# Performance work log

Hardware: AMD Instinct MI355X
Metric: run time of the kernel (lower is better)

## Reference

```python
import jax, jax.numpy as jnp
import numpy as np

N = 50000      # nodes
E = 800000     # edges
IN = 30        # atom features
H = 8          # attention heads
D = 32         # per-head out feats
G = 512        # graphs in batch
HID = 128      # predictor hidden
TASKS = 1
ALPHA = 0.2    # LeakyReLU slope
BN_EPS = 1e-5


def setup_inputs() -> dict:
    key = jax.random.key(0)
    ks = jax.random.split(key, 20)
    f = lambda k, shp: (jax.random.normal(k, shp, dtype=jnp.float32) * 0.1)
    return {
        'x': jax.random.normal(ks[0], (N, IN), dtype=jnp.float32),
        'src': jax.random.randint(ks[1], (E,), 0, N, dtype=jnp.int32),
        'dst': jax.random.randint(ks[2], (E,), 0, N, dtype=jnp.int32),
        'graph_ids': jnp.sort(jax.random.randint(ks[3], (N,), 0, G, dtype=jnp.int32)),
        # GAT layer 1 (in=30 -> 8 heads x 32, flatten + ELU, residual projection)
        'W1': f(ks[4], (IN, H * D)),
        'al1': f(ks[5], (H, D)),
        'ar1': f(ks[6], (H, D)),
        'b1': jnp.zeros((H * D,), jnp.float32),
        'resW1': f(ks[7], (IN, H * D)),
        # GAT layer 2 (in=256 -> 8 heads x 32, mean over heads, identity residual)
        'W2': f(ks[8], (H * D, H * D)),
        'al2': f(ks[9], (H, D)),
        'ar2': f(ks[10], (H, D)),
        'b2': jnp.zeros((H * D,), jnp.float32),
        # WeightedSumAndMax readout gate
        'Ww': f(ks[11], (D, 1)),
        'bw': jnp.zeros((1,), jnp.float32),
        # MLP predictor: Linear -> ReLU -> BatchNorm(eval) -> Linear
        'Wp1': f(ks[12], (2 * D, HID)),
        'bp1': jnp.zeros((HID,), jnp.float32),
        'gamma': jnp.ones((HID,), jnp.float32),
        'beta': jnp.zeros((HID,), jnp.float32),
        'rm': jnp.zeros((HID,), jnp.float32),
        'rv': jnp.ones((HID,), jnp.float32),
        'Wp2': f(ks[13], (HID, TASKS)),
        'bp2': jnp.zeros((TASKS,), jnp.float32),
    }


def _gat_layer(h, src, dst, W, al, ar, b):
    # h: [N, F_in] -> out: [N, H, D]
    n = h.shape[0]
    feat = (h @ W).reshape(n, H, D)                    # projected features
    el = jnp.sum(feat * al, axis=-1)                   # [N, H]
    er = jnp.sum(feat * ar, axis=-1)                   # [N, H]
    e = el[src] + er[dst]                              # [E, H]
    e = jnp.where(e > 0, e, ALPHA * e)                 # LeakyReLU
    m = jax.ops.segment_max(e, dst, num_segments=n)    # segment-softmax max
    m = jnp.where(jnp.isfinite(m), m, 0.0)             # guard empty segments
    ex = jnp.exp(e - m[dst])                           # [E, H]
    s = jax.ops.segment_sum(ex, dst, num_segments=n)   # [N, H]
    a = ex / jnp.maximum(s[dst], 1e-9)                 # normalized attention
    msg = a[:, :, None] * feat[src]                    # [E, H, D]
    out = jax.ops.segment_sum(msg, dst, num_segments=n)
    return out + b.reshape(1, H, D)


def reference(x, src, dst, graph_ids, W1, al1, ar1, b1, resW1,
              W2, al2, ar2, b2, Ww, bw, Wp1, bp1, gamma, beta, rm, rv, Wp2, bp2):
    # Layer 1: residual projection (in_feats != H*D), flatten heads, ELU
    h1 = _gat_layer(x, src, dst, W1, al1, ar1, b1)
    h1 = h1 + (x @ resW1).reshape(N, H, D)
    h1 = jax.nn.elu(h1.reshape(N, H * D))
    # Layer 2: identity residual (in_feats == H*D), mean over heads, no activation
    h2 = _gat_layer(h1, src, dst, W2, al2, ar2, b2)
    h2 = h2 + h1.reshape(N, H, D)
    h2 = jnp.mean(h2, axis=1)                          # [N, D]
    # WeightedSumAndMax readout
    w = jax.nn.sigmoid(h2 @ Ww + bw)                   # [N, 1]
    gsum = jax.ops.segment_sum(w * h2, graph_ids, num_segments=G)
    gmax = jax.ops.segment_max(h2, graph_ids, num_segments=G)
    gmax = jnp.where(jnp.isfinite(gmax), gmax, 0.0)
    g = jnp.concatenate([gsum, gmax], axis=-1)         # [G, 2D]
    # MLP predictor (eval-mode BatchNorm)
    p = jax.nn.relu(g @ Wp1 + bp1)
    p = (p - rm) / jnp.sqrt(rv + BN_EPS) * gamma + beta
    return p @ Wp2 + bp2                               # [G, TASKS]
```

## Files before the change

kernel.cpp:

```cpp
#include <hip/hip_runtime.h>
#include <math.h>

#define NN 50000
#define EE 800000
#define IN_F 30
#define NH 8
#define DH 32
#define HD 256
#define NG 512
#define NHID 128
#define ALPHA 0.2f
#define ENC_NEG_INF 0x007fffffu

#define SCAN_B 256
#define SCAN_NB ((NN + SCAN_B - 1)/SCAN_B)

typedef unsigned short u16;

__device__ __forceinline__ u16 f2bf(float f){
  unsigned u = __float_as_uint(f);
  u = u + 0x7FFFu + ((u >> 16) & 1u);
  return (u16)(u >> 16);
}
__device__ __forceinline__ float bf2f(u16 b){
  return __uint_as_float(((unsigned)b) << 16);
}
__device__ __forceinline__ float4 bf4_to_f4(ushort4 v){
  float4 r; r.x=bf2f(v.x); r.y=bf2f(v.y); r.z=bf2f(v.z); r.w=bf2f(v.w); return r;
}

__device__ __forceinline__ unsigned encf(float x){
  unsigned u = __float_as_uint(x);
  return (u & 0x80000000u) ? ~u : (u | 0x80000000u);
}
__device__ __forceinline__ float decf(unsigned u){
  return (u & 0x80000000u) ? __uint_as_float(u & 0x7fffffffu) : __uint_as_float(~u);
}

__global__ void k_init(int* counts, float* gsum, unsigned* gmax){
  int i = blockIdx.x*blockDim.x + threadIdx.x;
  if(i < NN) counts[i] = 0;
  if(i < NG*DH){ gsum[i] = 0.f; gmax[i] = ENC_NEG_INF; }
}

__global__ void k_hist(const int* __restrict__ dst, int* counts){
  int i = blockIdx.x*blockDim.x + threadIdx.x;
  if(i < EE) atomicAdd(&counts[dst[i]], 1);
}

__global__ void k_scan_partial(const int* __restrict__ counts, int* __restrict__ bsums){
  __shared__ int sd[SCAN_B];
  int b = blockIdx.x, t = threadIdx.x;
  int idx = b*SCAN_B + t;
  sd[t] = (idx<NN)? counts[idx] : 0;
  __syncthreads();
  for(int off=SCAN_B/2; off>0; off>>=1){
    if(t<off) sd[t] += sd[t+off];
    __syncthreads();
  }
  if(t==0) bsums[b] = sd[0];
}

__global__ void k_scan_bsums(int* bsums){
  __shared__ int sd[SCAN_B];
  int t = threadIdx.x;
  int v = (t<SCAN_NB)? bsums[t] : 0;
  sd[t]=v; __syncthreads();
  for(int off=1; off<SCAN_B; off<<=1){
    int u = (t>=off)? sd[t-off] : 0;
    __syncthreads();
    sd[t] += u;
    __syncthreads();
  }
  if(t<SCAN_NB) bsums[t] = sd[t]-v;
}

__global__ void k_scan_final(const int* __restrict__ counts, const int* __restrict__ bsums,
                             int* __restrict__ start, int* __restrict__ cursor){
  __shared__ int sd[SCAN_B];
  int b = blockIdx.x, t = threadIdx.x;
  int idx = b*SCAN_B + t;
  int v = (idx<NN)? counts[idx] : 0;
  sd[t]=v; __syncthreads();
  for(int off=1; off<SCAN_B; off<<=1){
    int u = (t>=off)? sd[t-off] : 0;
    __syncthreads();
    sd[t] += u;
    __syncthreads();
  }
  int ex = sd[t]-v + bsums[b];
  if(idx<NN){ start[idx]=ex; cursor[idx]=ex; }
}

__global__ void k_scatter(const int* __restrict__ dst, const int* __restrict__ src,
                          int* cursor, int* __restrict__ csr_src){
  int i = blockIdx.x*blockDim.x + threadIdx.x;
  if(i<EE){ int p = atomicAdd(&cursor[dst[i]],1); csr_src[p]=src[i]; }
}

#define TM1 16
__global__ void k_proj1(const float* __restrict__ x, const float* __restrict__ W1,
                        u16* __restrict__ feat16){
  __shared__ float xs[TM1][IN_F];
  int n0 = blockIdx.x*TM1;
  int t = threadIdx.x;
  for(int i=t;i<TM1*IN_F;i+=256){
    int m=i/IN_F, k=i-m*IN_F;
    xs[m][k] = x[(size_t)(n0+m)*IN_F+k];
  }
  __syncthreads();
  int jq = (t & 63) << 2;
  int m0 = t >> 6;
  float4 acc[4];
  #pragma unroll
  for(int r=0;r<4;r++){ acc[r].x=0.f; acc[r].y=0.f; acc[r].z=0.f; acc[r].w=0.f; }
  for(int k=0;k<IN_F;k++){
    float4 w = *(const float4*)&W1[k*HD + jq];
    #pragma unroll
    for(int r=0;r<4;r++){
      float xv = xs[m0 + (r<<2)][k];
      acc[r].x += xv*w.x; acc[r].y += xv*w.y; acc[r].z += xv*w.z; acc[r].w += xv*w.w;
    }
  }
  #pragma unroll
  for(int r=0;r<4;r++){
    int n = n0 + m0 + (r<<2);
    ushort4 o; o.x=f2bf(acc[r].x); o.y=f2bf(acc[r].y); o.z=f2bf(acc[r].z); o.w=f2bf(acc[r].w);
    *(ushort4*)&feat16[(size_t)n*HD + jq] = o;
  }
}

#define BM 64
#define BN 64
#define BK 16
#define LDP (BM+4)
__global__ void k_proj2(const float* __restrict__ X, const float* __restrict__ W,
                        u16* __restrict__ Y16){
  __shared__ float As[BK][LDP];
  __shared__ float Bs[BK][LDP];
  int t  = threadIdx.x;
  int tx = t & 15, ty = t >> 4;
  int n0 = blockIdx.x*BM;
  int c0 = blockIdx.y*BN;
  float acc[4][4];
  #pragma unroll
  for(int i=0;i<4;i++)
    #pragma unroll
    for(int j=0;j<4;j++) acc[i][j]=0.f;

  int am = t >> 2;
  int ak = (t & 3) << 2;
  int bk = t >> 4;
  int bn = (t & 15) << 2;

  for(int k0=0;k0<HD;k0+=BK){
    int n = n0 + am;
    float4 va = (n<NN) ? *(const float4*)&X[(size_t)n*HD + k0 + ak]
                       : make_float4(0.f,0.f,0.f,0.f);
    float4 vb = *(const float4*)&W[(size_t)(k0+bk)*HD + c0 + bn];
    __syncthreads();
    As[ak+0][am]=va.x; As[ak+1][am]=va.y; As[ak+2][am]=va.z; As[ak+3][am]=va.w;
    *(float4*)&Bs[bk][bn] = vb;
    __syncthreads();
    #pragma unroll
    for(int k=0;k<BK;k++){
      float4 a = *(const float4*)&As[k][ty<<2];
      float4 b = *(const float4*)&Bs[k][tx<<2];
      acc[0][0]+=a.x*b.x; acc[0][1]+=a.x*b.y; acc[0][2]+=a.x*b.z; acc[0][3]+=a.x*b.w;
      acc[1][0]+=a.y*b.x; acc[1][1]+=a.y*b.y; acc[1][2]+=a.y*b.z; acc[1][3]+=a.y*b.w;
      acc[2][0]+=a.z*b.x; acc[2][1]+=a.z*b.y; acc[2][2]+=a.z*b.z; acc[2][3]+=a.z*b.w;
      acc[3][0]+=a.w*b.x; acc[3][1]+=a.w*b.y; acc[3][2]+=a.w*b.z; acc[3][3]+=a.w*b.w;
    }
  }
  #pragma unroll
  for(int i=0;i<4;i++){
    int n = n0 + (ty<<2) + i;
    if(n<NN){
      ushort4 o; o.x=f2bf(acc[i][0]); o.y=f2bf(acc[i][1]); o.z=f2bf(acc[i][2]); o.w=f2bf(acc[i][3]);
      *(ushort4*)&Y16[(size_t)n*HD + c0 + (tx<<2)] = o;
    }
  }
}

__global__ void k_elr(const u16* __restrict__ feat16, const float* __restrict__ al,
                      const float* __restrict__ ar, float* __restrict__ el,
                      float* __restrict__ er){
  int i = blockIdx.x*blockDim.x + threadIdx.x;
  if(i >= NN*NH) return;
  int h = i & 7;
  const ushort4* f4 = (const ushort4*)(feat16 + (size_t)i*DH);
  const float4* a4 = (const float4*)(al + h*DH);
  const float4* b4 = (const float4*)(ar + h*DH);
  float ea=0.f, eb=0.f;
  #pragma unroll
  for(int q=0;q<8;q++){
    float4 f=bf4_to_f4(f4[q]); float4 a=a4[q], b=b4[q];
    ea += f.x*a.x + f.y*a.y + f.z*a.z + f.w*a.w;
    eb += f.x*b.x + f.y*b.y + f.z*b.z + f.w*b.w;
  }
  el[i]=ea; er[i]=eb;
}

__device__ __forceinline__ void gat_agg2(int n, int lane,
    const u16* __restrict__ feat16, const float* __restrict__ el,
    const float* __restrict__ er, const int* __restrict__ start,
    const int* __restrict__ counts, const int* __restrict__ csr_src,
    float* A, float& s_out){
  int half = lane >> 5;
  int l = lane & 31;
  int h = l >> 2;
  int col8 = l << 3;
  float erh = er[n*NH + h];
  int st = start[n], cnt = counts[n];
  float s = 0.f;
  #pragma unroll
  for(int j=0;j<8;j++) A[j]=0.f;
  for(int c=0; c<cnt; c+=64){
    int nrem = cnt - c;
    int lim = nrem < 64 ? nrem : 64;
    int myIdx = csr_src[st + c + (lane < lim ? lane : lim-1)];
    #pragma unroll 4
    for(int k=0; k<lim; k+=2){
      int sel = k + half;
      int sidx = __shfl(myIdx, sel, 64);
      float e = el[(size_t)sidx*NH + h] + erh;
      e = (e>0.f)? e : ALPHA*e;
      float w = (sel < lim) ? __expf(e) : 0.f;
      uint4 rv = *(const uint4*)&feat16[(size_t)sidx*HD + col8];
      float f0 = __uint_as_float(rv.x << 16);
      float f1 = __uint_as_float(rv.x & 0xffff0000u);
      float f2 = __uint_as_float(rv.y << 16);
      float f3 = __uint_as_float(rv.y & 0xffff0000u);
      float f4 = __uint_as_float(rv.z << 16);
      float f5 = __uint_as_float(rv.z & 0xffff0000u);
      float f6 = __uint_as_float(rv.w << 16);
      float f7 = __uint_as_float(rv.w & 0xffff0000u);
      s += w;
      A[0]+=w*f0; A[1]+=w*f1; A[2]+=w*f2; A[3]+=w*f3;
      A[4]+=w*f4; A[5]+=w*f5; A[6]+=w*f6; A[7]+=w*f7;
    }
  }
  s += __shfl_xor(s, 32, 64);
  #pragma unroll
  for(int j=0;j<8;j++) A[j] += __shfl_xor(A[j], 32, 64);
  float inv = 1.f/fmaxf(s, 1e-9f);
  #pragma unroll
  for(int j=0;j<8;j++) A[j] *= inv;
  s_out = s;
}

__global__ void k_gat1(const u16* __restrict__ feat16, const float* __restrict__ el,
    const float* __restrict__ er, const int* __restrict__ start,
    const int* __restrict__ counts, const int* __restrict__ csr_src,
    const float* __restrict__ x,
    const float* __restrict__ resW1, const float* __restrict__ b1,
    float* __restrict__ h1){
  int n = blockIdx.x*4 + (threadIdx.x>>6);
  int lane = threadIdx.x & 63;
  if(n>=NN) return;
  float A[8]; float s;
  gat_agg2(n,lane,feat16,el,er,start,counts,csr_src,A,s);
  int half = lane>>5, l = lane&31;
  int col8 = l<<3;
  float r[8];
  #pragma unroll
  for(int j=0;j<8;j++) r[j]=0.f;
  const float* xrow = x + (size_t)n*IN_F;
  int kb = half*15;
  #pragma unroll
  for(int k=0;k<15;k++){
    float xv = xrow[kb+k];
    const float4 w0 = *(const float4*)&resW1[(kb+k)*HD + col8];
    const float4 w1 = *(const float4*)&resW1[(kb+k)*HD + col8 + 4];
    r[0]+=xv*w0.x; r[1]+=xv*w0.y; r[2]+=xv*w0.z; r[3]+=xv*w0.w;
    r[4]+=xv*w1.x; r[5]+=xv*w1.y; r[6]+=xv*w1.z; r[7]+=xv*w1.w;
  }
  #pragma unroll
  for(int j=0;j<8;j++) r[j] += __shfl_xor(r[j], 32, 64);
  if(half==0){
    const float4 b0 = *(const float4*)&b1[col8];
    const float4 b4 = *(const float4*)&b1[col8+4];
    float4 o0, o1; float v;
    v = A[0]+r[0]+b0.x; o0.x = (v>0.f)? v : expf(v)-1.f;
    v = A[1]+r[1]+b0.y; o0.y = (v>0.f)? v : expf(v)-1.f;
    v = A[2]+r[2]+b0.z; o0.z = (v>0.f)? v : expf(v)-1.f;
    v = A[3]+r[3]+b0.w; o0.w = (v>0.f)? v : expf(v)-1.f;
    v = A[4]+r[4]+b4.x; o1.x = (v>0.f)? v : expf(v)-1.f;
    v = A[5]+r[5]+b4.y; o1.y = (v>0.f)? v : expf(v)-1.f;
    v = A[6]+r[6]+b4.z; o1.z = (v>0.f)? v : expf(v)-1.f;
    v = A[7]+r[7]+b4.w; o1.w = (v>0.f)? v : expf(v)-1.f;
    *(float4*)&h1[(size_t)n*HD + col8]     = o0;
    *(float4*)&h1[(size_t)n*HD + col8 + 4] = o1;
  }
}

__global__ void k_gat2(const u16* __restrict__ feat16, const float* __restrict__ el,
    const float* __restrict__ er, const int* __restrict__ start,
    const int* __restrict__ counts, const int* __restrict__ csr_src,
    const float* __restrict__ h1,
    const float* __restrict__ b2, float* __restrict__ h2){
  int n = blockIdx.x*4 + (threadIdx.x>>6);
  int lane = threadIdx.x & 63;
  if(n>=NN) return;
  float A[8]; float s;
  gat_agg2(n,lane,feat16,el,er,start,counts,csr_src,A,s);
  int l = lane&31;
  int col8 = l<<3;
  if(lane<32){
    const float4 b0 = *(const float4*)&b2[col8];
    const float4 b4 = *(const float4*)&b2[col8+4];
    const float4 h0 = *(const float4*)&h1[(size_t)n*HD + col8];
    const float4 h4 = *(const float4*)&h1[(size_t)n*HD + col8 + 4];
    float t[8];
    t[0]=A[0]+b0.x+h0.x; t[1]=A[1]+b0.y+h0.y; t[2]=A[2]+b0.z+h0.z; t[3]=A[3]+b0.w+h0.w;
    t[4]=A[4]+b4.x+h4.x; t[5]=A[5]+b4.y+h4.y; t[6]=A[6]+b4.z+h4.z; t[7]=A[7]+b4.w+h4.w;
    #pragma unroll
    for(int off=4; off<32; off<<=1){
      #pragma unroll
      for(int j=0;j<8;j++) t[j] += __shfl_xor(t[j], off, 64);
    }
    if(l<4){
      float4 o0, o1;
      o0.x=t[0]*0.125f; o0.y=t[1]*0.125f; o0.z=t[2]*0.125f; o0.w=t[3]*0.125f;
      o1.x=t[4]*0.125f; o1.y=t[5]*0.125f; o1.z=t[6]*0.125f; o1.w=t[7]*0.125f;
      *(float4*)&h2[(size_t)n*DH + (l<<3)]     = o0;
      *(float4*)&h2[(size_t)n*DH + (l<<3) + 4] = o1;
    }
  }
}

__global__ void k_gate(const float* __restrict__ h2, const float* __restrict__ Ww,
                       const float* __restrict__ bw, float* __restrict__ wgt){
  int n = blockIdx.x*blockDim.x + threadIdx.x;
  if(n>=NN) return;
  float acc = bw[0];
  const float4* hr = (const float4*)(h2 + (size_t)n*DH);
  const float4* w4 = (const float4*)Ww;
  #pragma unroll
  for(int q=0;q<8;q++){
    float4 h=hr[q], w=w4[q];
    acc += h.x*w.x + h.y*w.y + h.z*w.z + h.w*w.w;
  }
  wgt[n] = 1.f/(1.f+expf(-acc));
}

__global__ void k_readout(const float* __restrict__ h2, const float* __restrict__ wgt,
    const int* __restrict__ gid, float* gsum, unsigned* gmax){
  int i = blockIdx.x*blockDim.x + threadIdx.x;
  if(i>=NN*DH) return;
  int n = i>>5, d = i&31;
  int g = gid[n];
  float v = h2[i];
  atomicAdd(&gsum[g*DH+d], wgt[n]*v);
  atomicMax(&gmax[g*DH+d], encf(v));
}

__global__ void k_mlp(const float* __restrict__ gsum, const unsigned* __restrict__ gmax,
    const float* __restrict__ Wp1, const float* __restrict__ bp1,
    const float* __restrict__ gamma, const float* __restrict__ beta,
    const float* __restrict__ rm, const float* __restrict__ rv,
    const float* __restrict__ Wp2, const float* __restrict__ bp2,
    float* __restrict__ out){
  __shared__ float gs[2*DH];
  __shared__ float red[NHID];
  int g = blockIdx.x, t = threadIdx.x;
  if(t < DH) gs[t] = gsum[g*DH + t];
  else if(t < 2*DH){
    unsigned u = gmax[g*DH + (t-DH)];
    gs[t] = (u==ENC_NEG_INF)? 0.f : decf(u);
  }
  __syncthreads();
  float acc = bp1[t];
  #pragma unroll
  for(int k=0;k<2*DH;k++) acc += gs[k]*Wp1[k*NHID + t];
  acc = fmaxf(acc, 0.f);
  acc = (acc - rm[t])*rsqrtf(rv[t]+1e-5f)*gamma[t] + beta[t];
  red[t] = acc*Wp2[t];
  __syncthreads();
  for(int off=NHID/2; off>0; off>>=1){
    if(t<off) red[t] += red[t+off];
    __syncthreads();
  }
  if(t==0) out[g] = red[0] + bp2[0];
}

extern "C" void kernel_launch(void* const* d_in, const int* in_sizes, int n_in,
                              void* d_out, int out_size, void* d_ws, size_t ws_size,
                              hipStream_t stream){
  const float* x    = (const float*)d_in[0];
  const int*   src  = (const int*)  d_in[1];
  const int*   dst  = (const int*)  d_in[2];
  const int*   gid  = (const int*)  d_in[3];
  const float* W1   = (const float*)d_in[4];
  const float* al1  = (const float*)d_in[5];
  const float* ar1  = (const float*)d_in[6];
  const float* b1   = (const float*)d_in[7];
  const float* resW1= (const float*)d_in[8];
  const float* W2   = (const float*)d_in[9];
  const float* al2  = (const float*)d_in[10];
  const float* ar2  = (const float*)d_in[11];
  const float* b2   = (const float*)d_in[12];
  const float* Ww   = (const float*)d_in[13];
  const float* bw   = (const float*)d_in[14];
  const float* Wp1  = (const float*)d_in[15];
  const float* bp1  = (const float*)d_in[16];
  const float* gamma= (const float*)d_in[17];
  const float* beta = (const float*)d_in[18];
  const float* rm   = (const float*)d_in[19];
  const float* rv   = (const float*)d_in[20];
  const float* Wp2  = (const float*)d_in[21];
  const float* bp2  = (const float*)d_in[22];
  float* out = (float*)d_out;

  char* w = (char*)d_ws;
  u16*      feat16= (u16*)w;      w += (size_t)NN*HD*2;
  float*    h1    = (float*)w;    w += (size_t)NN*HD*4;
  float*    el    = (float*)w;    w += (size_t)NN*NH*4;
  float*    er    = (float*)w;    w += (size_t)NN*NH*4;
  float*    h2    = (float*)w;    w += (size_t)NN*DH*4;
  float*    wgt   = (float*)w;    w += (size_t)NN*4;
  float*    gsum  = (float*)w;    w += (size_t)NG*DH*4;
  unsigned* gmax  = (unsigned*)w; w += (size_t)NG*DH*4;
  int*      counts= (int*)w;      w += (size_t)NN*4;
  int*      start = (int*)w;      w += (size_t)NN*4;
  int*      cursor= (int*)w;      w += (size_t)NN*4;
  int*      bsums = (int*)w;      w += (size_t)SCAN_NB*4;
  int*      csr_src=(int*)w;      w += (size_t)EE*4;

  hipLaunchKernelGGL(k_init,         dim3((NN+255)/256),      dim3(256),    0, stream, counts, gsum, gmax);
  hipLaunchKernelGGL(k_hist,         dim3((EE+255)/256),      dim3(256),    0, stream, dst, counts);
  hipLaunchKernelGGL(k_scan_partial, dim3(SCAN_NB),           dim3(SCAN_B), 0, stream, counts, bsums);
  hipLaunchKernelGGL(k_scan_bsums,   dim3(1),                 dim3(SCAN_B), 0, stream, bsums);
  hipLaunchKernelGGL(k_scan_final,   dim3(SCAN_NB),           dim3(SCAN_B), 0, stream, counts, bsums, start, cursor);
  hipLaunchKernelGGL(k_scatter,      dim3((EE+255)/256),      dim3(256),    0, stream, dst, src, cursor, csr_src);
  hipLaunchKernelGGL(k_proj1,        dim3(NN/TM1),            dim3(256),    0, stream, x, W1, feat16);
  hipLaunchKernelGGL(k_elr,          dim3((NN*NH+255)/256),   dim3(256),    0, stream, feat16, al1, ar1, el, er);
  hipLaunchKernelGGL(k_gat1,         dim3((NN+3)/4),          dim3(256),    0, stream, feat16, el, er, start, counts, csr_src, x, resW1, b1, h1);
  hipLaunchKernelGGL(k_proj2,        dim3((NN+BM-1)/BM, HD/BN), dim3(256),  0, stream, h1, W2, feat16);
  hipLaunchKernelGGL(k_elr,          dim3((NN*NH+255)/256),   dim3(256),    0, stream, feat16, al2, ar2, el, er);
  hipLaunchKernelGGL(k_gat2,         dim3((NN+3)/4),          dim3(256),    0, stream, feat16, el, er, start, counts, csr_src, h1, b2, h2);
  hipLaunchKernelGGL(k_gate,         dim3((NN+255)/256),      dim3(256),    0, stream, h2, Ww, bw, wgt);
  hipLaunchKernelGGL(k_readout,      dim3((NN*DH+255)/256),   dim3(256),    0, stream, h2, wgt, gid, gsum, gmax);
  hipLaunchKernelGGL(k_mlp,          dim3(NG),                dim3(NHID),   0, stream, gsum, gmax, Wp1, bp1, gamma, beta, rm, rv, Wp2, bp2, out);
}
```

Before: 570.9 us.

## Precompute edge attention weights in CSR order and fuse readout into layer-2 aggregation

Adds a csr_dst array and a k_wts kernel that computes exp(LeakyReLU(el[src]+er[dst])) per edge and head into a CSR-ordered buffer. The aggregation loop then reads these weights instead of gathering el per neighbour and computing exp inline. The gate and readout kernels are folded into k_gat2, so h2 and wgt are no longer written and re-read. The cost is an extra 25.6 MB per-edge weight buffer that is written and read once per layer, plus atomics now issued from inside the aggregation kernel.

```diff
diff --git a/kernel.cpp b/kernel.cpp
--- a/kernel.cpp
+++ b/kernel.cpp
@@ -93,9 +93,26 @@
 }
 
 __global__ void k_scatter(const int* __restrict__ dst, const int* __restrict__ src,
-                          int* cursor, int* __restrict__ csr_src){
+                          int* cursor, int* __restrict__ csr_src, int* __restrict__ csr_dst){
   int i = blockIdx.x*blockDim.x + threadIdx.x;
-  if(i<EE){ int p = atomicAdd(&cursor[dst[i]],1); csr_src[p]=src[i]; }
+  if(i<EE){
+    int d = dst[i];
+    int p = atomicAdd(&cursor[d],1);
+    csr_src[p]=src[i];
+    csr_dst[p]=d;
+  }
+}
+
+__global__ void k_wts(const float* __restrict__ el, const float* __restrict__ er,
+                      const int* __restrict__ csr_src, const int* __restrict__ csr_dst,
+                      float* __restrict__ w_csr){
+  int i = blockIdx.x*blockDim.x + threadIdx.x;
+  if(i >= EE*NH) return;
+  int p = i>>3, h = i&7;
+  int s = csr_src[p], d = csr_dst[p];
+  float e = el[s*NH+h] + er[d*NH+h];
+  e = (e>0.f)? e : ALPHA*e;
+  w_csr[i] = __expf(e);
 }
 
 #define TM1 16
@@ -202,15 +219,13 @@
 }
 
 __device__ __forceinline__ void gat_agg2(int n, int lane,
-    const u16* __restrict__ feat16, const float* __restrict__ el,
-    const float* __restrict__ er, const int* __restrict__ start,
-    const int* __restrict__ counts, const int* __restrict__ csr_src,
-    float* A, float& s_out){
+    const u16* __restrict__ feat16, const float* __restrict__ w_csr,
+    const int* __restrict__ start, const int* __restrict__ counts,
+    const int* __restrict__ csr_src, float* A){
   int half = lane >> 5;
   int l = lane & 31;
   int h = l >> 2;
   int col8 = l << 3;
-  float erh = er[n*NH + h];
   int st = start[n], cnt = counts[n];
   float s = 0.f;
   #pragma unroll
@@ -223,9 +238,9 @@
     for(int k=0; k<lim; k+=2){
       int sel = k + half;
       int sidx = __shfl(myIdx, sel, 64);
-      float e = el[(size_t)sidx*NH + h] + erh;
-      e = (e>0.f)? e : ALPHA*e;
-      float w = (sel < lim) ? __expf(e) : 0.f;
+      int pcl = (sel < lim) ? sel : lim-1;
+      float wv = w_csr[(size_t)(st + c + pcl)*NH + h];
+      float w = (sel < lim) ? wv : 0.f;
       uint4 rv = *(const uint4*)&feat16[(size_t)sidx*HD + col8];
       float f0 = __uint_as_float(rv.x << 16);
       float f1 = __uint_as_float(rv.x & 0xffff0000u);
@@ -246,20 +261,18 @@
   float inv = 1.f/fmaxf(s, 1e-9f);
   #pragma unroll
   for(int j=0;j<8;j++) A[j] *= inv;
-  s_out = s;
-}
-
-__global__ void k_gat1(const u16* __restrict__ feat16, const float* __restrict__ el,
-    const float* __restrict__ er, const int* __restrict__ start,
-    const int* __restrict__ counts, const int* __restrict__ csr_src,
-    const float* __restrict__ x,
+}
+
+__global__ void k_gat1(const u16* __restrict__ feat16, const float* __restrict__ w_csr,
+    const int* __restrict__ start, const int* __restrict__ counts,
+    const int* __restrict__ csr_src, const float* __restrict__ x,
     const float* __restrict__ resW1, const float* __restrict__ b1,
     float* __restrict__ h1){
   int n = blockIdx.x*4 + (threadIdx.x>>6);
   int lane = threadIdx.x & 63;
   if(n>=NN) return;
-  float A[8]; float s;
-  gat_agg2(n,lane,feat16,el,er,start,counts,csr_src,A,s);
+  float A[8];
+  gat_agg2(n,lane,feat16,w_csr,start,counts,csr_src,A);
   int half = lane>>5, l = lane&31;
   int col8 = l<<3;
   float r[8];
@@ -294,16 +307,17 @@
   }
 }
 
-__global__ void k_gat2(const u16* __restrict__ feat16, const float* __restrict__ el,
-    const float* __restrict__ er, const int* __restrict__ start,
-    const int* __restrict__ counts, const int* __restrict__ csr_src,
-    const float* __restrict__ h1,
-    const float* __restrict__ b2, float* __restrict__ h2){
+__global__ void k_gat2(const u16* __restrict__ feat16, const float* __restrict__ w_csr,
+    const int* __restrict__ start, const int* __restrict__ counts,
+    const int* __restrict__ csr_src, const float* __restrict__ h1,
+    const float* __restrict__ b2, const int* __restrict__ gid,
+    const float* __restrict__ Ww, const float* __restrict__ bw,
+    float* gsum, unsigned* gmax){
   int n = blockIdx.x*4 + (threadIdx.x>>6);
   int lane = threadIdx.x & 63;
   if(n>=NN) return;
-  float A[8]; float s;
-  gat_agg2(n,lane,feat16,el,er,start,counts,csr_src,A,s);
+  float A[8];
+  gat_agg2(n,lane,feat16,w_csr,start,counts,csr_src,A);
   int l = lane&31;
   int col8 = l<<3;
   if(lane<32){
@@ -319,40 +333,26 @@
       #pragma unroll
       for(int j=0;j<8;j++) t[j] += __shfl_xor(t[j], off, 64);
     }
+    float vv[8]; float dotp = 0.f;
+    int dbase = (l & 3) << 3;
+    #pragma unroll
+    for(int j=0;j<8;j++){
+      vv[j] = t[j]*0.125f;
+      dotp += vv[j]*Ww[dbase + j];
+    }
+    dotp += __shfl_xor(dotp, 1, 64);
+    dotp += __shfl_xor(dotp, 2, 64);
+    float wg = 1.f/(1.f+__expf(-(dotp + bw[0])));
     if(l<4){
-      float4 o0, o1;
-      o0.x=t[0]*0.125f; o0.y=t[1]*0.125f; o0.z=t[2]*0.125f; o0.w=t[3]*0.125f;
-      o1.x=t[4]*0.125f; o1.y=t[5]*0.125f; o1.z=t[6]*0.125f; o1.w=t[7]*0.125f;
-      *(float4*)&h2[(size_t)n*DH + (l<<3)]     = o0;
-      *(float4*)&h2[(size_t)n*DH + (l<<3) + 4] = o1;
-    }
-  }
-}
-
-__global__ void k_gate(const float* __restrict__ h2, const float* __restrict__ Ww,
-                       const float* __restrict__ bw, float* __restrict__ wgt){
-  int n = blockIdx.x*blockDim.x + threadIdx.x;
-  if(n>=NN) return;
-  float acc = bw[0];
-  const float4* hr = (const float4*)(h2 + (size_t)n*DH);
-  const float4* w4 = (const float4*)Ww;
-  #pragma unroll
-  for(int q=0;q<8;q++){
-    float4 h=hr[q], w=w4[q];
-    acc += h.x*w.x + h.y*w.y + h.z*w.z + h.w*w.w;
-  }
-  wgt[n] = 1.f/(1.f+expf(-acc));
-}
-
-__global__ void k_readout(const float* __restrict__ h2, const float* __restrict__ wgt,
-    const int* __restrict__ gid, float* gsum, unsigned* gmax){
-  int i = blockIdx.x*blockDim.x + threadIdx.x;
-  if(i>=NN*DH) return;
-  int n = i>>5, d = i&31;
-  int g = gid[n];
-  float v = h2[i];
-  atomicAdd(&gsum[g*DH+d], wgt[n]*v);
-  atomicMax(&gmax[g*DH+d], encf(v));
+      int g = gid[n];
+      #pragma unroll
+      for(int j=0;j<8;j++){
+        int d = (l<<3)+j;
+        atomicAdd(&gsum[g*DH + d], wg*vv[j]);
+        atomicMax(&gmax[g*DH + d], encf(vv[j]));
+      }
+    }
+  }
 }
 
 __global__ void k_mlp(const float* __restrict__ gsum, const unsigned* __restrict__ gmax,
@@ -413,33 +413,33 @@
   float* out = (float*)d_out;
 
   char* w = (char*)d_ws;
-  u16*      feat16= (u16*)w;      w += (size_t)NN*HD*2;
-  float*    h1    = (float*)w;    w += (size_t)NN*HD*4;
-  float*    el    = (float*)w;    w += (size_t)NN*NH*4;
-  float*    er    = (float*)w;    w += (size_t)NN*NH*4;
-  float*    h2    = (float*)w;    w += (size_t)NN*DH*4;
-  float*    wgt   = (float*)w;    w += (size_t)NN*4;
-  float*    gsum  = (float*)w;    w += (size_t)NG*DH*4;
-  unsigned* gmax  = (unsigned*)w; w += (size_t)NG*DH*4;
-  int*      counts= (int*)w;      w += (size_t)NN*4;
-  int*      start = (int*)w;      w += (size_t)NN*4;
-  int*      cursor= (int*)w;      w += (size_t)NN*4;
-  int*      bsums = (int*)w;      w += (size_t)SCAN_NB*4;
-  int*      csr_src=(int*)w;      w += (size_t)EE*4;
-
-  hipLaunchKernelGGL(k_init,         dim3((NN+255)/256),      dim3(256),    0, stream, counts, gsum, gmax);
-  hipLaunchKernelGGL(k_hist,         dim3((EE+255)/256),      dim3(256),    0, stream, dst, counts);
-  hipLaunchKernelGGL(k_scan_partial, dim3(SCAN_NB),           dim3(SCAN_B), 0, stream, counts, bsums);
-  hipLaunchKernelGGL(k_scan_bsums,   dim3(1),                 dim3(SCAN_B), 0, stream, bsums);
-  hipLaunchKernelGGL(k_scan_final,   dim3(SCAN_NB),           dim3(SCAN_B), 0, stream, counts, bsums, start, cursor);
-  hipLaunchKernelGGL(k_scatter,      dim3((EE+255)/256),      dim3(256),    0, stream, dst, src, cursor, csr_src);
-  hipLaunchKernelGGL(k_proj1,        dim3(NN/TM1),            dim3(256),    0, stream, x, W1, feat16);
-  hipLaunchKernelGGL(k_elr,          dim3((NN*NH+255)/256),   dim3(256),    0, stream, feat16, al1, ar1, el, er);
-  hipLaunchKernelGGL(k_gat1,         dim3((NN+3)/4),          dim3(256),    0, stream, feat16, el, er, start, counts, csr_src, x, resW1, b1, h1);
-  hipLaunchKernelGGL(k_proj2,        dim3((NN+BM-1)/BM, HD/BN), dim3(256),  0, stream, h1, W2, feat16);
-  hipLaunchKernelGGL(k_elr,          dim3((NN*NH+255)/256),   dim3(256),    0, stream, feat16, al2, ar2, el, er);
-  hipLaunchKernelGGL(k_gat2,         dim3((NN+3)/4),          dim3(256),    0, stream, feat16, el, er, start, counts, csr_src, h1, b2, h2);
-  hipLaunchKernelGGL(k_gate,         dim3((NN+255)/256),      dim3(256),    0, stream, h2, Ww, bw, wgt);
-  hipLaunchKernelGGL(k_readout,      dim3((NN*DH+255)/256),   dim3(256),    0, stream, h2, wgt, gid, gsum, gmax);
-  hipLaunchKernelGGL(k_mlp,          dim3(NG),                dim3(NHID),   0, stream, gsum, gmax, Wp1, bp1, gamma, beta, rm, rv, Wp2, bp2, out);
-}
+  u16*      feat16 = (u16*)w;      w += (size_t)NN*HD*2;
+  float*    h1     = (float*)w;    w += (size_t)NN*HD*4;
+  float*    el     = (float*)w;    w += (size_t)NN*NH*4;
+  float*    er     = (float*)w;    w += (size_t)NN*NH*4;
+  float*    gsum   = (float*)w;    w += (size_t)NG*DH*4;
+  unsigned* gmax   = (unsigned*)w; w += (size_t)NG*DH*4;
+  int*      counts = (int*)w;      w += (size_t)NN*4;
+  int*      start  = (int*)w;      w += (size_t)NN*4;
+  int*      cursor = (int*)w;      w += (size_t)NN*4;
+  int*      bsums  = (int*)w;      w += (size_t)SCAN_NB*4;
+  int*      csr_src= (int*)w;      w += (size_t)EE*4;
+  int*      csr_dst= (int*)w;      w += (size_t)EE*4;
+  float*    w_csr  = (float*)w;    w += (size_t)EE*NH*4;
+
+  hipLaunchKernelGGL(k_init,         dim3((NN+255)/256),       dim3(256),    0, stream, counts, gsum, gmax);
+  hipLaunchKernelGGL(k_hist,         dim3((EE+255)/256),       dim3(256),    0, stream, dst, counts);
+  hipLaunchKernelGGL(k_scan_partial, dim3(SCAN_NB),            dim3(SCAN_B), 0, stream, counts, bsums);
+  hipLaunchKernelGGL(k_scan_bsums,   dim3(1),                  dim3(SCAN_B), 0, stream, bsums);
+  hipLaunchKernelGGL(k_scan_final,   dim3(SCAN_NB),            dim3(SCAN_B), 0, stream, counts, bsums, start, cursor);
+  hipLaunchKernelGGL(k_scatter,      dim3((EE+255)/256),       dim3(256),    0, stream, dst, src, cursor, csr_src, csr_dst);
+  hipLaunchKernelGGL(k_proj1,        dim3(NN/TM1),             dim3(256),    0, stream, x, W1, feat16);
+  hipLaunchKernelGGL(k_elr,          dim3((NN*NH+255)/256),    dim3(256),    0, stream, feat16, al1, ar1, el, er);
+  hipLaunchKernelGGL(k_wts,          dim3((EE*NH+255)/256),    dim3(256),    0, stream, el, er, csr_src, csr_dst, w_csr);
+  hipLaunchKernelGGL(k_gat1,         dim3((NN+3)/4),           dim3(256),    0, stream, feat16, w_csr, start, counts, csr_src, x, resW1, b1, h1);
+  hipLaunchKernelGGL(k_proj2,        dim3((NN+BM-1)/BM, HD/BN), dim3(256),   0, stream, h1, W2, feat16);
+  hipLaunchKernelGGL(k_elr,          dim3((NN*NH+255)/256),    dim3(256),    0, stream, feat16, al2, ar2, el, er);
+  hipLaunchKernelGGL(k_wts,          dim3((EE*NH+255)/256),    dim3(256),    0, stream, el, er, csr_src, csr_dst, w_csr);
+  hipLaunchKernelGGL(k_gat2,         dim3((NN+3)/4),           dim3(256),    0, stream, feat16, w_csr, start, counts, csr_src, h1, b2, gid, Ww, bw, gsum, gmax);
+  hipLaunchKernelGGL(k_mlp,          dim3(NG),                 dim3(NHID),   0, stream, gsum, gmax, Wp1, bp1, gamma, beta, rm, rv, Wp2, bp2, out);
+}
```

Measured after the change: 657.3 us. +15.1%, slower.

## Replace atomic graph readout with segmented per-graph block reduction using sorted graph ids

Applied to the files above, without the earlier changes.

Builds per-graph node counts and start offsets with a histogram and a single-block scan, relying on graph_ids being sorted so each graph's nodes are contiguous. The readout then runs one block per graph, computing the sigmoid gate inline and reducing sum and max in shared memory. This drops the separate gate kernel and the 1.6M global float and encoded-max atomics. In exchange it adds two small kernels, and correctness depends on graph ids being sorted, which the reference's setup guarantees.

```diff
diff --git a/kernel.cpp b/kernel.cpp
--- a/kernel.cpp
+++ b/kernel.cpp
@@ -10,7 +10,6 @@
 #define NG 512
 #define NHID 128
 #define ALPHA 0.2f
-#define ENC_NEG_INF 0x007fffffu
 
 #define SCAN_B 256
 #define SCAN_NB ((NN + SCAN_B - 1)/SCAN_B)
@@ -29,23 +28,34 @@
   float4 r; r.x=bf2f(v.x); r.y=bf2f(v.y); r.z=bf2f(v.z); r.w=bf2f(v.w); return r;
 }
 
-__device__ __forceinline__ unsigned encf(float x){
-  unsigned u = __float_as_uint(x);
-  return (u & 0x80000000u) ? ~u : (u | 0x80000000u);
-}
-__device__ __forceinline__ float decf(unsigned u){
-  return (u & 0x80000000u) ? __uint_as_float(u & 0x7fffffffu) : __uint_as_float(~u);
-}
-
-__global__ void k_init(int* counts, float* gsum, unsigned* gmax){
+__global__ void k_init(int* counts, int* gcounts){
   int i = blockIdx.x*blockDim.x + threadIdx.x;
   if(i < NN) counts[i] = 0;
-  if(i < NG*DH){ gsum[i] = 0.f; gmax[i] = ENC_NEG_INF; }
+  if(i < NG) gcounts[i] = 0;
 }
 
 __global__ void k_hist(const int* __restrict__ dst, int* counts){
   int i = blockIdx.x*blockDim.x + threadIdx.x;
   if(i < EE) atomicAdd(&counts[dst[i]], 1);
+}
+
+__global__ void k_ghist(const int* __restrict__ gid, int* gcounts){
+  int i = blockIdx.x*blockDim.x + threadIdx.x;
+  if(i < NN) atomicAdd(&gcounts[gid[i]], 1);
+}
+
+__global__ void k_gscan(const int* __restrict__ gcounts, int* __restrict__ gstart){
+  __shared__ int sd[NG];
+  int t = threadIdx.x;
+  int v = gcounts[t];
+  sd[t]=v; __syncthreads();
+  for(int off=1; off<NG; off<<=1){
+    int u = (t>=off)? sd[t-off] : 0;
+    __syncthreads();
+    sd[t] += u;
+    __syncthreads();
+  }
+  gstart[t] = sd[t]-v;
 }
 
 __global__ void k_scan_partial(const int* __restrict__ counts, int* __restrict__ bsums){
@@ -205,7 +215,7 @@
     const u16* __restrict__ feat16, const float* __restrict__ el,
     const float* __restrict__ er, const int* __restrict__ start,
     const int* __restrict__ counts, const int* __restrict__ csr_src,
-    float* A, float& s_out){
+    float* A){
   int half = lane >> 5;
   int l = lane & 31;
   int h = l >> 2;
@@ -246,7 +256,6 @@
   float inv = 1.f/fmaxf(s, 1e-9f);
   #pragma unroll
   for(int j=0;j<8;j++) A[j] *= inv;
-  s_out = s;
 }
 
 __global__ void k_gat1(const u16* __restrict__ feat16, const float* __restrict__ el,
@@ -258,8 +267,8 @@
   int n = blockIdx.x*4 + (threadIdx.x>>6);
   int lane = threadIdx.x & 63;
   if(n>=NN) return;
-  float A[8]; float s;
-  gat_agg2(n,lane,feat16,el,er,start,counts,csr_src,A,s);
+  float A[8];
+  gat_agg2(n,lane,feat16,el,er,start,counts,csr_src,A);
   int half = lane>>5, l = lane&31;
   int col8 = l<<3;
   float r[8];
@@ -302,8 +311,8 @@
   int n = blockIdx.x*4 + (threadIdx.x>>6);
   int lane = threadIdx.x & 63;
   if(n>=NN) return;
-  float A[8]; float s;
-  gat_agg2(n,lane,feat16,el,er,start,counts,csr_src,A,s);
+  float A[8];
+  gat_agg2(n,lane,feat16,el,er,start,counts,csr_src,A);
   int l = lane&31;
   int col8 = l<<3;
   if(lane<32){
@@ -329,33 +338,44 @@
   }
 }
 
-__global__ void k_gate(const float* __restrict__ h2, const float* __restrict__ Ww,
-                       const float* __restrict__ bw, float* __restrict__ wgt){
-  int n = blockIdx.x*blockDim.x + threadIdx.x;
-  if(n>=NN) return;
-  float acc = bw[0];
-  const float4* hr = (const float4*)(h2 + (size_t)n*DH);
-  const float4* w4 = (const float4*)Ww;
-  #pragma unroll
-  for(int q=0;q<8;q++){
-    float4 h=hr[q], w=w4[q];
-    acc += h.x*w.x + h.y*w.y + h.z*w.z + h.w*w.w;
-  }
-  wgt[n] = 1.f/(1.f+expf(-acc));
-}
-
-__global__ void k_readout(const float* __restrict__ h2, const float* __restrict__ wgt,
-    const int* __restrict__ gid, float* gsum, unsigned* gmax){
-  int i = blockIdx.x*blockDim.x + threadIdx.x;
-  if(i>=NN*DH) return;
-  int n = i>>5, d = i&31;
-  int g = gid[n];
-  float v = h2[i];
-  atomicAdd(&gsum[g*DH+d], wgt[n]*v);
-  atomicMax(&gmax[g*DH+d], encf(v));
-}
-
-__global__ void k_mlp(const float* __restrict__ gsum, const unsigned* __restrict__ gmax,
+__global__ void k_readout(const float* __restrict__ h2, const float* __restrict__ Ww,
+    const float* __restrict__ bw, const int* __restrict__ gstart,
+    const int* __restrict__ gcounts, float* __restrict__ gsum,
+    float* __restrict__ gmaxf){
+  __shared__ float ssum[8][DH];
+  __shared__ float smax[8][DH];
+  int g = blockIdx.x;
+  int t = threadIdx.x;
+  int half = (t & 63) >> 5;
+  int wid = t >> 6;
+  int l = t & 31;
+  int rg = wid*2 + half;
+  int s = gstart[g], cnt = gcounts[g];
+  float w_d = Ww[l];
+  float bw0 = bw[0];
+  float sum = 0.f, mx = -INFINITY;
+  for(int r = rg; r < cnt; r += 8){
+    float v = h2[(size_t)(s+r)*DH + l];
+    float p = v*w_d;
+    p += __shfl_xor(p,1,64); p += __shfl_xor(p,2,64); p += __shfl_xor(p,4,64);
+    p += __shfl_xor(p,8,64); p += __shfl_xor(p,16,64);
+    float wg = 1.f/(1.f+__expf(-(p+bw0)));
+    sum += wg*v;
+    mx = fmaxf(mx, v);
+  }
+  ssum[rg][l] = sum;
+  smax[rg][l] = mx;
+  __syncthreads();
+  if(t < DH){
+    float a = 0.f, m = -INFINITY;
+    #pragma unroll
+    for(int r=0;r<8;r++){ a += ssum[r][t]; m = fmaxf(m, smax[r][t]); }
+    gsum[g*DH+t]  = a;
+    gmaxf[g*DH+t] = isfinite(m)? m : 0.f;
+  }
+}
+
+__global__ void k_mlp(const float* __restrict__ gsum, const float* __restrict__ gmaxf,
     const float* __restrict__ Wp1, const float* __restrict__ bp1,
     const float* __restrict__ gamma, const float* __restrict__ beta,
     const float* __restrict__ rm, const float* __restrict__ rv,
@@ -365,10 +385,7 @@
   __shared__ float red[NHID];
   int g = blockIdx.x, t = threadIdx.x;
   if(t < DH) gs[t] = gsum[g*DH + t];
-  else if(t < 2*DH){
-    unsigned u = gmax[g*DH + (t-DH)];
-    gs[t] = (u==ENC_NEG_INF)? 0.f : decf(u);
-  }
+  else if(t < 2*DH) gs[t] = gmaxf[g*DH + (t-DH)];
   __syncthreads();
   float acc = bp1[t];
   #pragma unroll
@@ -413,33 +430,35 @@
   float* out = (float*)d_out;
 
   char* w = (char*)d_ws;
-  u16*      feat16= (u16*)w;      w += (size_t)NN*HD*2;
-  float*    h1    = (float*)w;    w += (size_t)NN*HD*4;
-  float*    el    = (float*)w;    w += (size_t)NN*NH*4;
-  float*    er    = (float*)w;    w += (size_t)NN*NH*4;
-  float*    h2    = (float*)w;    w += (size_t)NN*DH*4;
-  float*    wgt   = (float*)w;    w += (size_t)NN*4;
-  float*    gsum  = (float*)w;    w += (size_t)NG*DH*4;
-  unsigned* gmax  = (unsigned*)w; w += (size_t)NG*DH*4;
-  int*      counts= (int*)w;      w += (size_t)NN*4;
-  int*      start = (int*)w;      w += (size_t)NN*4;
-  int*      cursor= (int*)w;      w += (size_t)NN*4;
-  int*      bsums = (int*)w;      w += (size_t)SCAN_NB*4;
-  int*      csr_src=(int*)w;      w += (size_t)EE*4;
-
-  hipLaunchKernelGGL(k_init,         dim3((NN+255)/256),      dim3(256),    0, stream, counts, gsum, gmax);
-  hipLaunchKernelGGL(k_hist,         dim3((EE+255)/256),      dim3(256),    0, stream, dst, counts);
-  hipLaunchKernelGGL(k_scan_partial, dim3(SCAN_NB),           dim3(SCAN_B), 0, stream, counts, bsums);
-  hipLaunchKernelGGL(k_scan_bsums,   dim3(1),                 dim3(SCAN_B), 0, stream, bsums);
-  hipLaunchKernelGGL(k_scan_final,   dim3(SCAN_NB),           dim3(SCAN_B), 0, stream, counts, bsums, start, cursor);
-  hipLaunchKernelGGL(k_scatter,      dim3((EE+255)/256),      dim3(256),    0, stream, dst, src, cursor, csr_src);
-  hipLaunchKernelGGL(k_proj1,        dim3(NN/TM1),            dim3(256),    0, stream, x, W1, feat16);
-  hipLaunchKernelGGL(k_elr,          dim3((NN*NH+255)/256),   dim3(256),    0, stream, feat16, al1, ar1, el, er);
-  hipLaunchKernelGGL(k_gat1,         dim3((NN+3)/4),          dim3(256),    0, stream, feat16, el, er, start, counts, csr_src, x, resW1, b1, h1);
-  hipLaunchKernelGGL(k_proj2,        dim3((NN+BM-1)/BM, HD/BN), dim3(256),  0, stream, h1, W2, feat16);
-  hipLaunchKernelGGL(k_elr,          dim3((NN*NH+255)/256),   dim3(256),    0, stream, feat16, al2, ar2, el, er);
-  hipLaunchKernelGGL(k_gat2,         dim3((NN+3)/4),          dim3(256),    0, stream, feat16, el, er, start, counts, csr_src, h1, b2, h2);
-  hipLaunchKernelGGL(k_gate,         dim3((NN+255)/256),      dim3(256),    0, stream, h2, Ww, bw, wgt);
-  hipLaunchKernelGGL(k_readout,      dim3((NN*DH+255)/256),   dim3(256),    0, stream, h2, wgt, gid, gsum, gmax);
-  hipLaunchKernelGGL(k_mlp,          dim3(NG),                dim3(NHID),   0, stream, gsum, gmax, Wp1, bp1, gamma, beta, rm, rv, Wp2, bp2, out);
-}
+  u16*      feat16 = (u16*)w;      w += (size_t)NN*HD*2;
+  float*    h1     = (float*)w;    w += (size_t)NN*HD*4;
+  float*    el     = (float*)w;    w += (size_t)NN*NH*4;
+  float*    er     = (float*)w;    w += (size_t)NN*NH*4;
+  float*    h2     = (float*)w;    w += (size_t)NN*DH*4;
+  float*    gsum   = (float*)w;    w += (size_t)NG*DH*4;
+  float*    gmaxf  = (float*)w;    w += (size_t)NG*DH*4;
+  int*      counts = (int*)w;      w += (size_t)NN*4;
+  int*      start  = (int*)w;      w += (size_t)NN*4;
+  int*      cursor = (int*)w;      w += (size_t)NN*4;
+  int*      bsums  = (int*)w;      w += (size_t)SCAN_NB*4;
+  int*      gcounts= (int*)w;      w += (size_t)NG*4;
+  int*      gstart = (int*)w;      w += (size_t)NG*4;
+  int*      csr_src= (int*)w;      w += (size_t)EE*4;
+
+  hipLaunchKernelGGL(k_init,         dim3((NN+255)/256),       dim3(256),    0, stream, counts, gcounts);
+  hipLaunchKernelGGL(k_hist,         dim3((EE+255)/256),       dim3(256),    0, stream, dst, counts);
+  hipLaunchKernelGGL(k_ghist,        dim3((NN+255)/256),       dim3(256),    0, stream, gid, gcounts);
+  hipLaunchKernelGGL(k_gscan,        dim3(1),                  dim3(NG),     0, stream, gcounts, gstart);
+  hipLaunchKernelGGL(k_scan_partial, dim3(SCAN_NB),            dim3(SCAN_B), 0, stream, counts, bsums);
+  hipLaunchKernelGGL(k_scan_bsums,   dim3(1),                  dim3(SCAN_B), 0, stream, bsums);
+  hipLaunchKernelGGL(k_scan_final,   dim3(SCAN_NB),            dim3(SCAN_B), 0, stream, counts, bsums, start, cursor);
+  hipLaunchKernelGGL(k_scatter,      dim3((EE+255)/256),       dim3(256),    0, stream, dst, src, cursor, csr_src);
+  hipLaunchKernelGGL(k_proj1,        dim3(NN/TM1),             dim3(256),    0, stream, x, W1, feat16);
+  hipLaunchKernelGGL(k_elr,          dim3((NN*NH+255)/256),    dim3(256),    0, stream, feat16, al1, ar1, el, er);
+  hipLaunchKernelGGL(k_gat1,         dim3((NN+3)/4),           dim3(256),    0, stream, feat16, el, er, start, counts, csr_src, x, resW1, b1, h1);
+  hipLaunchKernelGGL(k_proj2,        dim3((NN+BM-1)/BM, HD/BN), dim3(256),   0, stream, h1, W2, feat16);
+  hipLaunchKernelGGL(k_elr,          dim3((NN*NH+255)/256),    dim3(256),    0, stream, feat16, al2, ar2, el, er);
+  hipLaunchKernelGGL(k_gat2,         dim3((NN+3)/4),           dim3(256),    0, stream, feat16, el, er, start, counts, csr_src, h1, b2, h2);
+  hipLaunchKernelGGL(k_readout,      dim3(NG),                 dim3(256),    0, stream, h2, Ww, bw, gstart, gcounts, gsum, gmaxf);
+  hipLaunchKernelGGL(k_mlp,          dim3(NG),                 dim3(NHID),   0, stream, gsum, gmaxf, Wp1, bp1, gamma, beta, rm, rv, Wp2, bp2, out);
+}
```

New measurement: 562.4 us. No clear change (-1.5%).
